# Performance work log

Measured on AMD Instinct MI355X. Metric: run time of the kernel, lower is better.

## Reference

```python
import jax, jax.numpy as jnp
import numpy as np

B = 4000        # graphs
N = 64          # atoms (nodes) per graph; also conv1 in_channels (Linear(num_atoms, 64))
C = 64          # hidden / out channels (hard-coded 64 in ChargeModel)
E_PER = 512     # edges per graph (avg degree 8)
NT = B * N      # total nodes


def setup_inputs() -> dict:
    key = jax.random.key(0)
    ks = jax.random.split(key, 10)
    x = jax.random.normal(ks[0], (NT, N), dtype=jnp.float32)
    # block-local random edges: each graph's edges stay inside its node block
    off = (jnp.arange(B, dtype=jnp.int32) * N)[:, None]
    src = (jax.random.randint(ks[1], (B, E_PER), 0, N, dtype=jnp.int32) + off).reshape(-1)
    dst = (jax.random.randint(ks[2], (B, E_PER), 0, N, dtype=jnp.int32) + off).reshape(-1)
    edge_index = jnp.stack([src, dst], axis=0)  # [2, B*E_PER]
    s = 1.0 / jnp.sqrt(jnp.float32(C))  # keep activations O(1) across 3 layers
    W1 = jax.random.normal(ks[3], (N, C), dtype=jnp.float32) * s
    W2 = jax.random.normal(ks[4], (C, C), dtype=jnp.float32) * s
    W3 = jax.random.normal(ks[5], (C, C), dtype=jnp.float32) * s
    b1 = jax.random.normal(ks[6], (C,), dtype=jnp.float32) * 0.1
    b2 = jax.random.normal(ks[7], (C,), dtype=jnp.float32) * 0.1
    b3 = jax.random.normal(ks[8], (C,), dtype=jnp.float32) * 0.1
    return {"x": x, "edge_index": edge_index, "W1": W1, "b1": b1,
            "W2": W2, "b2": b2, "W3": W3, "b3": b3}


def reference(x, edge_index, W1, b1, W2, b2, W3, b3):
    nt = x.shape[0]
    src, dst = edge_index[0], edge_index[1]
    loops = jnp.arange(nt, dtype=src.dtype)
    row = jnp.concatenate([src, loops])  # self-loops appended (add_self_loops)
    col = jnp.concatenate([dst, loops])
    # degree of target nodes (col), shared across the three layers
    deg = jax.ops.segment_sum(jnp.ones(row.shape[0], dtype=x.dtype), col, num_segments=nt)
    dinv = jnp.where(deg > 0, jax.lax.rsqrt(jnp.maximum(deg, 1e-12)), 0.0)
    norm = dinv[row] * dinv[col]  # [E']

    def gcn(h, W, b):
        h = h @ W                                   # linear (no bias in lin)
        msg = norm[:, None] * h[row]                # message: norm * x_j
        out = jax.ops.segment_sum(msg, col, num_segments=nt)  # aggr='add'
        return out + b

    h = gcn(x, W1, b1)
    h = gcn(h, W2, b2)
    h = gcn(h, W3, b3)
    # per-graph readout: mean over nodes and channels -> one scalar per graph
    y = h.reshape(B, N, C).mean(axis=(1, 2))
    return y
```

## Files before the change

kernel.cpp:

```cpp
#include <hip/hip_runtime.h>

#define NG      4000
#define EPG     512
#define CSTRIDE 35

__global__ __launch_bounds__(256) void prep_vec(
    const float* __restrict__ W1, const float* __restrict__ b1,
    const float* __restrict__ W2, const float* __restrict__ b2,
    const float* __restrict__ W3, const float* __restrict__ b3,
    float* __restrict__ out)
{
    __shared__ float M[4096];
    __shared__ float w3[64], q2[64];
    const int t = threadIdx.x;
    const int row = t >> 2, q = t & 3;

    for (int i = t; i < 1024; i += 256) ((float4*)M)[i] = ((const float4*)W3)[i];
    __syncthreads();
    {
        float acc = 0.f;
        #pragma unroll
        for (int i = 0; i < 16; ++i) acc += M[row * 64 + q * 16 + i];
        acc += __shfl_down(acc, 2, 4);
        acc += __shfl_down(acc, 1, 4);
        if (q == 0) w3[row] = acc;
    }
    __syncthreads();

    for (int i = t; i < 1024; i += 256) ((float4*)M)[i] = ((const float4*)W2)[i];
    __syncthreads();
    {
        float acc = 0.f;
        #pragma unroll
        for (int i = 0; i < 16; ++i) {
            const int c = q * 16 + i;
            acc += M[row * 64 + c] * w3[c];
        }
        acc += __shfl_down(acc, 2, 4);
        acc += __shfl_down(acc, 1, 4);
        if (q == 0) q2[row] = acc;
    }
    __syncthreads();

    for (int i = t; i < 1024; i += 256) ((float4*)M)[i] = ((const float4*)W1)[i];
    __syncthreads();
    {
        float acc = 0.f;
        #pragma unroll
        for (int i = 0; i < 16; ++i) {
            const int c = q * 16 + i;
            acc += M[row * 64 + c] * q2[c];
        }
        acc += __shfl_down(acc, 2, 4);
        acc += __shfl_down(acc, 1, 4);
        if (q == 0) out[row] = acc;
    }

    if (t < 64) {
        float t1 = b1[t] * q2[t];
        float t2 = b2[t] * w3[t];
        float t3 = b3[t];
        #pragma unroll
        for (int off = 32; off > 0; off >>= 1) {
            t1 += __shfl_down(t1, off, 64);
            t2 += __shfl_down(t2, off, 64);
            t3 += __shfl_down(t3, off, 64);
        }
        if (t == 0) { out[64] = t1; out[65] = t2; out[66] = 64.f * t3; }
    }
}

__global__ __launch_bounds__(256, 4) void gcn3_collapse(
    const float* __restrict__ x, const int* __restrict__ ei,
    const float* __restrict__ pv, float* __restrict__ y, int etot)
{
    __shared__ int   Cnt[64 * CSTRIDE];
    __shared__ int   deg[64];
    __shared__ float dinv[64], zd[64], u1[64], u2[64], u3[64], xp[64];

    const int g = blockIdx.x, t = threadIdx.x;
    const int base = g * 64;
    const int row = t >> 2, q4 = t & 3;

    const float4* xg = (const float4*)(x + (size_t)g * 4096 + row * 64 + q4 * 16);
    const float4 xr0 = xg[0], xr1 = xg[1], xr2 = xg[2], xr3 = xg[3];

    const float4* pp = (const float4*)(pv + q4 * 16);
    const float4 p0 = pp[0], p1 = pp[1], p2 = pp[2], p3 = pp[3];

    const int2 sv = *(const int2*)(ei + (size_t)g * EPG + 2 * t);
    const int2 dv = *(const int2*)(ei + (size_t)etot + (size_t)g * EPG + 2 * t);

    {
        const int4 z = {0, 0, 0, 0};
        int4* c4 = (int4*)Cnt;
        #pragma unroll 1
        for (int i = t; i < (64 * CSTRIDE) / 4; i += 256) c4[i] = z;
        if (t < 64) deg[t] = 0;
    }
    __syncthreads();

    {
        const int sa = sv.x - base, da = dv.x - base;
        const int sb = sv.y - base, db = dv.y - base;
        atomicAdd(&deg[da], 1);
        atomicAdd(&deg[db], 1);
        atomicAdd(&Cnt[sa * CSTRIDE + (da >> 1)], 1 << ((da & 1) * 16));
        atomicAdd(&Cnt[sb * CSTRIDE + (db >> 1)], 1 << ((db & 1) * 16));
    }

    {
        float part = xr0.x * p0.x + xr0.y * p0.y + xr0.z * p0.z + xr0.w * p0.w
                   + xr1.x * p1.x + xr1.y * p1.y + xr1.z * p1.z + xr1.w * p1.w
                   + xr2.x * p2.x + xr2.y * p2.y + xr2.z * p2.z + xr2.w * p2.w
                   + xr3.x * p3.x + xr3.y * p3.y + xr3.z * p3.z + xr3.w * p3.w;
        part += __shfl_down(part, 2, 4);
        part += __shfl_down(part, 1, 4);
        if (q4 == 0) xp[row] = part;
    }
    __syncthreads();

    if (t < 64) {
        const float di = rsqrtf((float)(deg[t] + 1));
        dinv[t] = di;
        zd[t] = di;
    }
    __syncthreads();

    auto upass = [&](float* u, const float* zprev) {
        const int* rp = Cnt + row * CSTRIDE + q4 * 8;
        float acc = 0.f;
        #pragma unroll
        for (int i = 0; i < 8; ++i) {
            const unsigned v = (unsigned)rp[i];
            const int d0 = q4 * 16 + 2 * i;
            acc += (float)(v & 0xffffu) * zd[d0];
            acc += (float)(v >> 16)     * zd[d0 + 1];
        }
        acc += __shfl_down(acc, 2, 4);
        acc += __shfl_down(acc, 1, 4);
        if (q4 == 0) {
            const float di = dinv[row];
            const float zp = zprev ? zprev[row] : 1.0f;
            u[row] = di * acc + di * di * zp;
        }
    };

    upass(u1, nullptr);
    __syncthreads();
    if (t < 64) zd[t] = dinv[t] * u1[t];
    __syncthreads();
    upass(u2, u1);
    __syncthreads();
    if (t < 64) zd[t] = dinv[t] * u2[t];
    __syncthreads();
    upass(u3, u2);
    __syncthreads();

    if (t < 64) {
        float r  = u3[t] * xp[t];
        float a1 = u1[t];
        float a2 = u2[t];
        #pragma unroll
        for (int off = 32; off > 0; off >>= 1) {
            r  += __shfl_down(r,  off, 64);
            a1 += __shfl_down(a1, off, 64);
            a2 += __shfl_down(a2, off, 64);
        }
        if (t == 0) {
            const float beta1 = pv[64], beta2 = pv[65], beta3 = pv[66];
            y[g] = (r + a2 * beta1 + a1 * beta2 + beta3) * (1.0f / 4096.0f);
        }
    }
}

extern "C" void kernel_launch(void* const* d_in, const int* in_sizes, int n_in,
                              void* d_out, int out_size, void* d_ws, size_t ws_size,
                              hipStream_t stream) {
    const float* x  = (const float*)d_in[0];
    const int*   ei = (const int*)  d_in[1];
    const float* W1 = (const float*)d_in[2];
    const float* b1 = (const float*)d_in[3];
    const float* W2 = (const float*)d_in[4];
    const float* b2 = (const float*)d_in[5];
    const float* W3 = (const float*)d_in[6];
    const float* b3 = (const float*)d_in[7];
    float* y = (float*)d_out;
    const int etot = in_sizes[1] / 2;

    float* pv = (float*)d_ws;
    hipLaunchKernelGGL(prep_vec, dim3(1), dim3(256), 0, stream,
                       W1, b1, W2, b2, W3, b3, pv);
    hipLaunchKernelGGL(gcn3_collapse, dim3(NG), dim3(256), 0, stream,
                       x, ei, pv, y, etot);
}
```

Before: 27.47 us.

## Process one graph per wavefront with float atomics instead of count matrix

Maps each graph to a single 64-lane wavefront, four graphs per block, so the per-graph work needs no __syncthreads barriers. The packed adjacency count matrix and its matrix-vector passes are replaced by direct float atomicAdd scatter over the edges held in registers in each of the three passes. It drops the LDS zeroing and block-wide barriers in exchange for more LDS atomics and heavier register use (16 float4 of x per lane). Correctness relies on implicit wavefront lockstep ordering of LDS accesses with no explicit barriers, which is fragile.

```diff
diff --git a/kernel.cpp b/kernel.cpp
--- a/kernel.cpp
+++ b/kernel.cpp
@@ -1,8 +1,7 @@
 #include <hip/hip_runtime.h>
 
-#define NG      4000
-#define EPG     512
-#define CSTRIDE 35
+#define NG  4000
+#define EPG 512
 
 __global__ __launch_bounds__(256) void prep_vec(
     const float* __restrict__ W1, const float* __restrict__ b1,
@@ -70,107 +69,81 @@
     }
 }
 
-__global__ __launch_bounds__(256, 4) void gcn3_collapse(
+__global__ __launch_bounds__(256, 4) void gcn3_wave(
     const float* __restrict__ x, const int* __restrict__ ei,
     const float* __restrict__ pv, float* __restrict__ y, int etot)
 {
-    __shared__ int   Cnt[64 * CSTRIDE];
-    __shared__ int   deg[64];
-    __shared__ float dinv[64], zd[64], u1[64], u2[64], u3[64], xp[64];
+    __shared__ float s_zd [4][64];
+    __shared__ float s_acc[4][64];
+    __shared__ int   s_deg[4][64];
+    __shared__ float s_p  [4][64];
 
-    const int g = blockIdx.x, t = threadIdx.x;
+    const int t = threadIdx.x, w = t >> 6, lane = t & 63;
+    const int g = blockIdx.x * 4 + w;
     const int base = g * 64;
-    const int row = t >> 2, q4 = t & 3;
 
-    const float4* xg = (const float4*)(x + (size_t)g * 4096 + row * 64 + q4 * 16);
-    const float4 xr0 = xg[0], xr1 = xg[1], xr2 = xg[2], xr3 = xg[3];
+    float* zd  = s_zd [w];
+    float* acc = s_acc[w];
+    int*   deg = s_deg[w];
+    float* pl  = s_p  [w];
 
-    const float4* pp = (const float4*)(pv + q4 * 16);
-    const float4 p0 = pp[0], p1 = pp[1], p2 = pp[2], p3 = pp[3];
+    const float4* xg = (const float4*)(x + (size_t)g * 4096);
+    float4 xr[16];
+    #pragma unroll
+    for (int k = 0; k < 16; ++k) xr[k] = xg[lane + 64 * k];
 
-    const int2 sv = *(const int2*)(ei + (size_t)g * EPG + 2 * t);
-    const int2 dv = *(const int2*)(ei + (size_t)etot + (size_t)g * EPG + 2 * t);
+    const int4* sp = (const int4*)(ei + (size_t)g * EPG);
+    const int4* dp = (const int4*)(ei + (size_t)etot + (size_t)g * EPG);
+    const int4 sA = sp[lane], sB = sp[lane + 64];
+    const int4 dA = dp[lane], dB = dp[lane + 64];
 
-    {
-        const int4 z = {0, 0, 0, 0};
-        int4* c4 = (int4*)Cnt;
-        #pragma unroll 1
-        for (int i = t; i < (64 * CSTRIDE) / 4; i += 256) c4[i] = z;
-        if (t < 64) deg[t] = 0;
-    }
-    __syncthreads();
+    pl[lane]  = pv[lane];
+    deg[lane] = 0;
 
-    {
-        const int sa = sv.x - base, da = dv.x - base;
-        const int sb = sv.y - base, db = dv.y - base;
-        atomicAdd(&deg[da], 1);
-        atomicAdd(&deg[db], 1);
-        atomicAdd(&Cnt[sa * CSTRIDE + (da >> 1)], 1 << ((da & 1) * 16));
-        atomicAdd(&Cnt[sb * CSTRIDE + (db >> 1)], 1 << ((db & 1) * 16));
+    int se[8], de[8];
+    se[0] = sA.x - base; se[1] = sA.y - base; se[2] = sA.z - base; se[3] = sA.w - base;
+    se[4] = sB.x - base; se[5] = sB.y - base; se[6] = sB.z - base; se[7] = sB.w - base;
+    de[0] = dA.x - base; de[1] = dA.y - base; de[2] = dA.z - base; de[3] = dA.w - base;
+    de[4] = dB.x - base; de[5] = dB.y - base; de[6] = dB.z - base; de[7] = dB.w - base;
+
+    #pragma unroll
+    for (int e = 0; e < 8; ++e) atomicAdd(&deg[de[e]], 1);
+    const float dr = rsqrtf((float)(deg[lane] + 1));
+
+    float zprev = 1.f;
+    float u1, u2, u3;
+    #pragma unroll
+    for (int pass = 0; pass < 3; ++pass) {
+        zd[lane]  = dr * zprev;
+        acc[lane] = 0.f;
+        #pragma unroll
+        for (int e = 0; e < 8; ++e)
+            atomicAdd(&acc[se[e]], zd[de[e]]);
+        const float u = dr * acc[lane] + dr * dr * zprev;
+        if (pass == 0) u1 = u; else if (pass == 1) u2 = u; else u3 = u;
+        zprev = u;
     }
 
-    {
-        float part = xr0.x * p0.x + xr0.y * p0.y + xr0.z * p0.z + xr0.w * p0.w
-                   + xr1.x * p1.x + xr1.y * p1.y + xr1.z * p1.z + xr1.w * p1.w
-                   + xr2.x * p2.x + xr2.y * p2.y + xr2.z * p2.z + xr2.w * p2.w
-                   + xr3.x * p3.x + xr3.y * p3.y + xr3.z * p3.z + xr3.w * p3.w;
-        part += __shfl_down(part, 2, 4);
-        part += __shfl_down(part, 1, 4);
-        if (q4 == 0) xp[row] = part;
+    zd[lane] = u3;
+    const float4 p4 = *(const float4*)&pl[(lane & 15) * 4];
+    float partial = 0.f;
+    #pragma unroll
+    for (int k = 0; k < 16; ++k) {
+        const float u3v = zd[(lane >> 4) + 4 * k];
+        partial += u3v * (xr[k].x * p4.x + xr[k].y * p4.y +
+                          xr[k].z * p4.z + xr[k].w * p4.w);
     }
-    __syncthreads();
 
-    if (t < 64) {
-        const float di = rsqrtf((float)(deg[t] + 1));
-        dinv[t] = di;
-        zd[t] = di;
+    float r = partial, a1 = u1, a2 = u2;
+    #pragma unroll
+    for (int off = 32; off > 0; off >>= 1) {
+        r  += __shfl_down(r,  off, 64);
+        a1 += __shfl_down(a1, off, 64);
+        a2 += __shfl_down(a2, off, 64);
     }
-    __syncthreads();
-
-    auto upass = [&](float* u, const float* zprev) {
-        const int* rp = Cnt + row * CSTRIDE + q4 * 8;
-        float acc = 0.f;
-        #pragma unroll
-        for (int i = 0; i < 8; ++i) {
-            const unsigned v = (unsigned)rp[i];
-            const int d0 = q4 * 16 + 2 * i;
-            acc += (float)(v & 0xffffu) * zd[d0];
-            acc += (float)(v >> 16)     * zd[d0 + 1];
-        }
-        acc += __shfl_down(acc, 2, 4);
-        acc += __shfl_down(acc, 1, 4);
-        if (q4 == 0) {
-            const float di = dinv[row];
-            const float zp = zprev ? zprev[row] : 1.0f;
-            u[row] = di * acc + di * di * zp;
-        }
-    };
-
-    upass(u1, nullptr);
-    __syncthreads();
-    if (t < 64) zd[t] = dinv[t] * u1[t];
-    __syncthreads();
-    upass(u2, u1);
-    __syncthreads();
-    if (t < 64) zd[t] = dinv[t] * u2[t];
-    __syncthreads();
-    upass(u3, u2);
-    __syncthreads();
-
-    if (t < 64) {
-        float r  = u3[t] * xp[t];
-        float a1 = u1[t];
-        float a2 = u2[t];
-        #pragma unroll
-        for (int off = 32; off > 0; off >>= 1) {
-            r  += __shfl_down(r,  off, 64);
-            a1 += __shfl_down(a1, off, 64);
-            a2 += __shfl_down(a2, off, 64);
-        }
-        if (t == 0) {
-            const float beta1 = pv[64], beta2 = pv[65], beta3 = pv[66];
-            y[g] = (r + a2 * beta1 + a1 * beta2 + beta3) * (1.0f / 4096.0f);
-        }
+    if (lane == 0) {
+        const float beta1 = pv[64], beta2 = pv[65], beta3 = pv[66];
+        y[g] = (r + a2 * beta1 + a1 * beta2 + beta3) * (1.0f / 4096.0f);
     }
 }
 
@@ -191,6 +164,6 @@
     float* pv = (float*)d_ws;
     hipLaunchKernelGGL(prep_vec, dim3(1), dim3(256), 0, stream,
                        W1, b1, W2, b2, W3, b3, pv);
-    hipLaunchKernelGGL(gcn3_collapse, dim3(NG), dim3(256), 0, stream,
+    hipLaunchKernelGGL(gcn3_wave, dim3(NG / 4), dim3(256), 0, stream,
                        x, ei, pv, y, etot);
 }
```

Result: slower. 48.67 us (+77.2%).
